# Kernel optimization log

Measured on AMD Instinct MI355X. Metric: run time of the kernel, lower is better.

The kernel has to match this reference:

```python
import jax, jax.numpy as jnp
import numpy as np

H = 1024
S = 2048
B = 16

def setup_inputs() -> dict:
    key = jax.random.key(0)
    k1, k2, k3, k4, k5, k6 = jax.random.split(key, 6)
    hidden = jax.random.normal(k1, (1, B, H), dtype=jnp.float32)
    encoder_outputs = jax.random.normal(k2, (S, B, H), dtype=jnp.float32)
    seq_mask = jax.random.randint(k3, (B, S), 0, 2, dtype=jnp.int32)
    # nn.Linear(2H, H): weight [H, 2H], bias [H]
    lim1 = 1.0 / np.sqrt(2 * H)
    attn_w = jax.random.uniform(k4, (H, 2 * H), minval=-lim1, maxval=lim1, dtype=jnp.float32)
    attn_b = jax.random.uniform(k5, (H,), minval=-lim1, maxval=lim1, dtype=jnp.float32)
    # nn.Linear(H, 1, bias=False): weight [1, H]
    lim2 = 1.0 / np.sqrt(H)
    score_w = jax.random.uniform(k6, (1, H), minval=-lim2, maxval=lim2, dtype=jnp.float32)
    return {"hidden": hidden, "encoder_outputs": encoder_outputs, "seq_mask": seq_mask,
            "attn_w": attn_w, "attn_b": attn_b, "score_w": score_w}

def reference(hidden, encoder_outputs, seq_mask, attn_w, attn_b, score_w):
    # Faithful to: cat([hidden.repeat(S,1,1), encoder_outputs], -1) @ attn_w.T + attn_b
    # Split the concat-linear into two GEMMs (identical math, avoids the big concat).
    h = hidden.shape[-1]
    Wh = attn_w[:, :h]   # acts on repeated hidden
    We = attn_w[:, h:]   # acts on encoder outputs
    # hidden: [1,B,H] broadcasts over S; encoder_outputs: [S,B,H]
    pre = jnp.einsum('obh,kh->obk', hidden, Wh) + jnp.einsum('sbh,kh->sbk', encoder_outputs, We) + attn_b
    proj = jnp.tanh(pre)                               # [S,B,H]
    energies = jnp.einsum('sbh,oh->sbo', proj, score_w)[..., 0]  # [S,B]
    energies = energies.T                              # [B,S] (transpose(0,1) in original)
    energies = jnp.where(seq_mask.astype(bool), jnp.float32(-1e12), energies)
    attn = jax.nn.softmax(energies, axis=1)            # [B,S]
    return attn[:, None, :]                            # [B,1,S]
```

## Files before the change

### kernel.cpp

```cpp
#include <hip/hip_runtime.h>
#include <hip/hip_bf16.h>

#define HDIM 1024
#define SEQ 2048
#define BATCH 16
#define M_TOT (SEQ*BATCH)
#define NBLK 4
#define BM 256
#define BN 256
#define BKT 64
#define NT (HDIM/BKT)

#define NB_ENC ((M_TOT*HDIM)/(8*256))
#define NB_WE  ((HDIM*HDIM)/(8*256))
#define NB_QK  (HDIM)

typedef __attribute__((ext_vector_type(8))) short short8;
typedef __attribute__((ext_vector_type(4))) float f32x4;

typedef const void __attribute__((address_space(1))) gvoid_t;
typedef void __attribute__((address_space(3))) svoid_t;
#define GLD16(gp, lp) __builtin_amdgcn_global_load_lds((gvoid_t*)(gp), (svoid_t*)(lp), 16, 0, 0)
#define VMC(N) asm volatile("s_waitcnt vmcnt(" #N ")" ::: "memory")

static __device__ __forceinline__ unsigned short f2bf(float f) {
    unsigned int x = __float_as_uint(f);
    unsigned int r = (x + 0x7FFFu + ((x >> 16) & 1u)) >> 16;
    return (unsigned short)r;
}

__global__ __launch_bounds__(256) void prep_all(const float* __restrict__ hidden,
                                                const float* __restrict__ enc,
                                                const float* __restrict__ attn_w,
                                                const float* __restrict__ attn_b,
                                                float* __restrict__ q,
                                                __hip_bfloat16* __restrict__ web,
                                                __hip_bfloat16* __restrict__ encb) {
    int bid = blockIdx.x;
    if (bid < NB_ENC) {
        size_t i0 = ((size_t)bid * 256 + threadIdx.x) * 8;
        const float4* s = reinterpret_cast<const float4*>(enc + i0);
        float4 a = s[0], b = s[1];
        union { unsigned short u[8]; short8 v; } cv;
        cv.u[0] = f2bf(a.x); cv.u[1] = f2bf(a.y); cv.u[2] = f2bf(a.z); cv.u[3] = f2bf(a.w);
        cv.u[4] = f2bf(b.x); cv.u[5] = f2bf(b.y); cv.u[6] = f2bf(b.z); cv.u[7] = f2bf(b.w);
        *reinterpret_cast<short8*>((unsigned short*)encb + i0) = cv.v;
        return;
    }
    if (bid < NB_ENC + NB_WE) {
        size_t i0 = ((size_t)(bid - NB_ENC) * 256 + threadIdx.x) * 8;
        int n = (int)(i0 >> 10);
        int h = (int)(i0 & 1023);
        const float4* src = reinterpret_cast<const float4*>(attn_w + (size_t)n * (2 * HDIM) + HDIM + h);
        float4 a = src[0], b = src[1];
        union { unsigned short u[8]; short8 v; } cv;
        cv.u[0] = f2bf(a.x); cv.u[1] = f2bf(a.y); cv.u[2] = f2bf(a.z); cv.u[3] = f2bf(a.w);
        cv.u[4] = f2bf(b.x); cv.u[5] = f2bf(b.y); cv.u[6] = f2bf(b.z); cv.u[7] = f2bf(b.w);
        *reinterpret_cast<short8*>((unsigned short*)web + i0) = cv.v;
        return;
    }
    int k = bid - (NB_ENC + NB_WE);
    int tid = threadIdx.x;
    const float* w = attn_w + (size_t)k * (2 * HDIM);
    float p[BATCH];
#pragma unroll
    for (int b = 0; b < BATCH; b++) p[b] = 0.f;
    for (int h = tid; h < HDIM; h += 256) {
        float wv = w[h];
#pragma unroll
        for (int b = 0; b < BATCH; b++) p[b] += hidden[b * HDIM + h] * wv;
    }
#pragma unroll
    for (int b = 0; b < BATCH; b++) {
        for (int off = 32; off; off >>= 1) p[b] += __shfl_down(p[b], off);
    }
    __shared__ float red[4][BATCH];
    int lane = tid & 63, wid = tid >> 6;
    if (lane == 0) {
#pragma unroll
        for (int b = 0; b < BATCH; b++) red[wid][b] = p[b];
    }
    __syncthreads();
    if (tid < BATCH) {
        float s = red[0][tid] + red[1][tid] + red[2][tid] + red[3][tid] + attn_b[k];
        q[(size_t)tid * HDIM + k] = s;
    }
}

__global__ __launch_bounds__(512, 2) void gemm8(const __hip_bfloat16* __restrict__ encb,
                                                const __hip_bfloat16* __restrict__ web,
                                                const float* __restrict__ qv,
                                                const float* __restrict__ score_w,
                                                float* __restrict__ part) {
    __shared__ __align__(16) char pool[163840];

    int tid = threadIdx.x;
    int lane = tid & 63;
    int wid = tid >> 6;
    int wr = wid >> 2;
    int wc = wid & 3;

    int bid = blockIdx.x;
    int lin = (bid & 7) * 64 + (bid >> 3);
    int bm = lin >> 2;
    int bn = lin & 3;
    int m0 = bm * BM, n0 = bn * BN;

    int srow = tid >> 3;
    int scolb = (((tid & 7) ^ ((tid >> 3) & 7)) << 4);
    const char* eb = (const char*)encb;
    const char* wb = (const char*)web;

    auto STG = [&](const char* g, int ldsoff) {
        GLD16(g + (size_t)srow * 2048 + scolb, pool + ldsoff + wid * 1024);
        GLD16(g + (size_t)(srow + 64) * 2048 + scolb, pool + ldsoff + 8192 + wid * 1024);
    };
    auto APTR = [&](int kt, int h) { return eb + ((size_t)(m0 + h * 128) * HDIM + kt * BKT) * 2; };
    auto BPTR = [&](int kt, int h) { return wb + ((size_t)(n0 + h * 128) * HDIM + kt * BKT) * 2; };
#define ALDS(par, h) ((par) * 32768 + (h) * 16384)
#define BLDS(buf, h) (65536 + (buf) * 32768 + (h) * 16384)

    int lq = lane & 15, lh = lane >> 4;
    int flip = (lane & 7) << 4;
    int pks0 = lq * 128 + ((lh * 16) ^ flip);
    int pks1 = lq * 128 + (((64 + lh * 16)) ^ flip);
    int aFB = wr * 16384;
    int bOFF = (wc >> 1) * 16384 + (wc & 1) * 8192;

    f32x4 acc[8][4];
#pragma unroll
    for (int i = 0; i < 8; i++)
#pragma unroll
        for (int j = 0; j < 4; j++) acc[i][j] = (f32x4)0.f;
    short8 br[4][2];

#define RD8(off) (*reinterpret_cast<const short8*>(pool + (off)))

#define CLUSTER(Q, PAR, BB, STAGE_STMT)                                                   \
    {                                                                                     \
        if ((Q) == 0) {                                                                   \
            _Pragma("unroll") for (int nj = 0; nj < 4; ++nj) {                            \
                br[nj][0] = RD8(65536 + (BB) * 32768 + bOFF + nj * 2048 + pks0);          \
                br[nj][1] = RD8(65536 + (BB) * 32768 + bOFF + nj * 2048 + pks1);          \
            }                                                                             \
        }                                                                                 \
        short8 a0k0 = RD8(aFB + (PAR) * 32768 + (2 * (Q)) * 2048 + pks0);                 \
        short8 a0k1 = RD8(aFB + (PAR) * 32768 + (2 * (Q)) * 2048 + pks1);                 \
        short8 a1k0 = RD8(aFB + (PAR) * 32768 + (2 * (Q) + 1) * 2048 + pks0);             \
        short8 a1k1 = RD8(aFB + (PAR) * 32768 + (2 * (Q) + 1) * 2048 + pks1);             \
        STAGE_STMT;                                                                       \
        __builtin_amdgcn_s_setprio(1);                                                    \
        _Pragma("unroll") for (int nj = 0; nj < 4; ++nj) {                                \
            acc[2 * (Q)][nj] = __builtin_amdgcn_mfma_f32_16x16x32_bf16(a0k0, br[nj][0], acc[2 * (Q)][nj], 0, 0, 0); \
            acc[2 * (Q)][nj] = __builtin_amdgcn_mfma_f32_16x16x32_bf16(a0k1, br[nj][1], acc[2 * (Q)][nj], 0, 0, 0); \
            acc[2 * (Q) + 1][nj] = __builtin_amdgcn_mfma_f32_16x16x32_bf16(a1k0, br[nj][0], acc[2 * (Q) + 1][nj], 0, 0, 0); \
            acc[2 * (Q) + 1][nj] = __builtin_amdgcn_mfma_f32_16x16x32_bf16(a1k1, br[nj][1], acc[2 * (Q) + 1][nj], 0, 0, 0); \
        }                                                                                 \
        __builtin_amdgcn_s_setprio(0);                                                    \
    }

#define TILE(PAR, BB, S1, S2, S3, S4, CLOSE)                                              \
    {                                                                                     \
        CLUSTER(0, PAR, BB, S1);                                                          \
        CLUSTER(1, PAR, BB, S2);                                                          \
        CLUSTER(2, PAR, BB, S3);                                                          \
        CLUSTER(3, PAR, BB, S4);                                                          \
        CLOSE;                                                                            \
        __builtin_amdgcn_s_barrier();                                                     \
        __builtin_amdgcn_sched_barrier(0);                                                \
    }

    STG(APTR(0, 0), ALDS(0, 0));
    STG(APTR(0, 1), ALDS(0, 1));
    STG(BPTR(0, 0), BLDS(0, 0));
    STG(BPTR(0, 1), BLDS(0, 1));
    STG(BPTR(1, 0), BLDS(1, 0));
    STG(BPTR(1, 1), BLDS(1, 1));
    VMC(4);
    __builtin_amdgcn_s_barrier();
    __builtin_amdgcn_sched_barrier(0);

#pragma unroll 1
    for (int J = 0; J < 2; ++J) {
        int t = 6 * J;
        TILE(0, 0, STG(APTR(t + 1, 0), ALDS(1, 0)), STG(APTR(t + 1, 1), ALDS(1, 1)),
                   STG(BPTR(t + 2, 0), BLDS(2, 0)), STG(BPTR(t + 2, 1), BLDS(2, 1)), VMC(4));
        TILE(1, 1, STG(APTR(t + 2, 0), ALDS(0, 0)), STG(APTR(t + 2, 1), ALDS(0, 1)),
                   STG(BPTR(t + 3, 0), BLDS(0, 0)), STG(BPTR(t + 3, 1), BLDS(0, 1)), VMC(4));
        TILE(0, 2, STG(APTR(t + 3, 0), ALDS(1, 0)), STG(APTR(t + 3, 1), ALDS(1, 1)),
                   STG(BPTR(t + 4, 0), BLDS(1, 0)), STG(BPTR(t + 4, 1), BLDS(1, 1)), VMC(4));
        TILE(1, 0, STG(APTR(t + 4, 0), ALDS(0, 0)), STG(APTR(t + 4, 1), ALDS(0, 1)),
                   STG(BPTR(t + 5, 0), BLDS(2, 0)), STG(BPTR(t + 5, 1), BLDS(2, 1)), VMC(4));
        TILE(0, 1, STG(APTR(t + 5, 0), ALDS(1, 0)), STG(APTR(t + 5, 1), ALDS(1, 1)),
                   STG(BPTR(t + 6, 0), BLDS(0, 0)), STG(BPTR(t + 6, 1), BLDS(0, 1)), VMC(4));
        TILE(1, 2, STG(APTR(t + 6, 0), ALDS(0, 0)), STG(APTR(t + 6, 1), ALDS(0, 1)),
                   STG(BPTR(t + 7, 0), BLDS(1, 0)), STG(BPTR(t + 7, 1), BLDS(1, 1)), VMC(4));
    }
    TILE(0, 0, STG(APTR(13, 0), ALDS(1, 0)), STG(APTR(13, 1), ALDS(1, 1)),
               STG(BPTR(14, 0), BLDS(2, 0)), STG(BPTR(14, 1), BLDS(2, 1)), VMC(4));
    TILE(1, 1, STG(APTR(14, 0), ALDS(0, 0)), STG(APTR(14, 1), ALDS(0, 1)),
               STG(BPTR(15, 0), BLDS(0, 0)), STG(BPTR(15, 1), BLDS(0, 1)), VMC(4));
    TILE(0, 2, STG(APTR(15, 0), ALDS(1, 0)), STG(APTR(15, 1), ALDS(1, 1)), , , VMC(0));
    TILE(1, 0, , , , , );

    float* q_lds = reinterpret_cast<float*>(pool);
    float* sc_lds = reinterpret_cast<float*>(pool + 16384);
    float* eng = reinterpret_cast<float*>(pool + 17408);
    {
        int qb = tid >> 5;
        int kl = (tid & 31) * 8;
        const float4* src = reinterpret_cast<const float4*>(qv + (size_t)qb * HDIM + n0 + kl);
        float4 v0 = src[0], v1 = src[1];
        *reinterpret_cast<float4*>(&q_lds[qb * 256 + kl]) = v0;
        *reinterpret_cast<float4*>(&q_lds[qb * 256 + kl + 4]) = v1;
        if (tid < BN) sc_lds[tid] = score_w[n0 + tid];
    }
    __syncthreads();

#pragma unroll
    for (int mi = 0; mi < 8; ++mi) {
#pragma unroll
        for (int r = 0; r < 4; ++r) {
            int b = lh * 4 + r;
            float s = 0.f;
#pragma unroll
            for (int nj = 0; nj < 4; ++nj) {
                int kl = wc * 64 + nj * 16 + lq;
                float v = acc[mi][nj][r] + q_lds[b * 256 + kl];
                float t = 1.f - 2.f / (__expf(2.f * v) + 1.f);
                s += sc_lds[kl] * t;
            }
            for (int off = 1; off < 16; off <<= 1) s += __shfl_xor(s, off);
            if (lq == 0) eng[wc * 256 + wr * 128 + mi * 16 + b] = s;
        }
    }
    __syncthreads();
    if (tid < BM) {
        float s = eng[tid] + eng[256 + tid] + eng[512 + tid] + eng[768 + tid];
        part[(size_t)bn * M_TOT + m0 + tid] = s;
    }
#undef CLUSTER
#undef TILE
#undef RD8
#undef ALDS
#undef BLDS
}

__global__ __launch_bounds__(256) void softmax_kernel(const float* __restrict__ part,
                                                      const int* __restrict__ mask,
                                                      float* __restrict__ out) {
    int b = blockIdx.x;
    int tid = threadIdx.x;
    __shared__ float e_lds[SEQ];
    __shared__ float red[4], red2[4];
    int lane = tid & 63, wid = tid >> 6;
    float lmax = -3.4e38f;
    for (int it = 0; it < SEQ / 256; ++it) {
        int s = it * 256 + tid;
        size_t m = (size_t)s * BATCH + b;
        float e = 0.f;
#pragma unroll
        for (int c = 0; c < NBLK; c++) e += part[(size_t)c * M_TOT + m];
        if (mask[(size_t)b * SEQ + s]) e = -1e12f;
        e_lds[s] = e;
        lmax = fmaxf(lmax, e);
    }
    for (int off = 32; off; off >>= 1) lmax = fmaxf(lmax, __shfl_xor(lmax, off));
    if (lane == 0) red[wid] = lmax;
    __syncthreads();
    float gmax = fmaxf(fmaxf(red[0], red[1]), fmaxf(red[2], red[3]));
    float lsum = 0.f;
    for (int it = 0; it < SEQ / 256; ++it) {
        int s = it * 256 + tid;
        float p = __expf(e_lds[s] - gmax);
        e_lds[s] = p;
        lsum += p;
    }
    for (int off = 32; off; off >>= 1) lsum += __shfl_xor(lsum, off);
    if (lane == 0) red2[wid] = lsum;
    __syncthreads();
    float inv = 1.f / (red2[0] + red2[1] + red2[2] + red2[3]);
    for (int it = 0; it < SEQ / 256; ++it) {
        int s = it * 256 + tid;
        out[(size_t)b * SEQ + s] = e_lds[s] * inv;
    }
}

extern "C" void kernel_launch(void* const* d_in, const int* in_sizes, int n_in,
                              void* d_out, int out_size, void* d_ws, size_t ws_size,
                              hipStream_t stream) {
    const float* hidden   = (const float*)d_in[0];
    const float* enc      = (const float*)d_in[1];
    const int*   seq_mask = (const int*)d_in[2];
    const float* attn_w   = (const float*)d_in[3];
    const float* attn_b   = (const float*)d_in[4];
    const float* score_w  = (const float*)d_in[5];
    float* out = (float*)d_out;

    char* ws = (char*)d_ws;
    float* q = (float*)ws;
    __hip_bfloat16* web = (__hip_bfloat16*)(ws + 65536);
    float* part = (float*)(ws + 65536 + 2 * 1024 * 1024);
    __hip_bfloat16* encb = (__hip_bfloat16*)(ws + 65536 + 3 * 1024 * 1024);

    prep_all<<<dim3(NB_ENC + NB_WE + NB_QK), dim3(256), 0, stream>>>(hidden, enc, attn_w, attn_b, q, web, encb);
    gemm8<<<dim3(NBLK * (M_TOT / BM)), dim3(512), 0, stream>>>(encb, web, q, score_w, part);
    softmax_kernel<<<dim3(BATCH), dim3(256), 0, stream>>>(part, seq_mask, out);
}
```

Measured before the change: 118.6 us.

## Fuse fp32-to-bf16 encoder conversion into GEMM A-tile loading

Drops the separate pass that converts encoder_outputs to a bf16 workspace copy. The GEMM now loads fp32 A tiles into registers, converts them to bf16 and writes them into swizzled LDS, and keeps the async global-to-LDS path only for the weight tiles. This removes a full write and re-read of the 64MB bf16 copy. BM is halved to 128 and the grid doubled, so each block holds fewer accumulators and uses less LDS. The cost is more register pressure and extra VALU conversion work inside the main loop, and weight tiles are reused less per block.

```diff
diff --git a/kernel.cpp b/kernel.cpp
--- a/kernel.cpp
+++ b/kernel.cpp
@@ -6,12 +6,11 @@
 #define BATCH 16
 #define M_TOT (SEQ*BATCH)
 #define NBLK 4
-#define BM 256
+#define BM 128
 #define BN 256
 #define BKT 64
 #define NT (HDIM/BKT)
 
-#define NB_ENC ((M_TOT*HDIM)/(8*256))
 #define NB_WE  ((HDIM*HDIM)/(8*256))
 #define NB_QK  (HDIM)
 
@@ -22,6 +21,7 @@
 typedef void __attribute__((address_space(3))) svoid_t;
 #define GLD16(gp, lp) __builtin_amdgcn_global_load_lds((gvoid_t*)(gp), (svoid_t*)(lp), 16, 0, 0)
 #define VMC(N) asm volatile("s_waitcnt vmcnt(" #N ")" ::: "memory")
+#define LGKM0 asm volatile("s_waitcnt lgkmcnt(0)" ::: "memory")
 
 static __device__ __forceinline__ unsigned short f2bf(float f) {
     unsigned int x = __float_as_uint(f);
@@ -30,25 +30,13 @@
 }
 
 __global__ __launch_bounds__(256) void prep_all(const float* __restrict__ hidden,
-                                                const float* __restrict__ enc,
                                                 const float* __restrict__ attn_w,
                                                 const float* __restrict__ attn_b,
                                                 float* __restrict__ q,
-                                                __hip_bfloat16* __restrict__ web,
-                                                __hip_bfloat16* __restrict__ encb) {
+                                                __hip_bfloat16* __restrict__ web) {
     int bid = blockIdx.x;
-    if (bid < NB_ENC) {
+    if (bid < NB_WE) {
         size_t i0 = ((size_t)bid * 256 + threadIdx.x) * 8;
-        const float4* s = reinterpret_cast<const float4*>(enc + i0);
-        float4 a = s[0], b = s[1];
-        union { unsigned short u[8]; short8 v; } cv;
-        cv.u[0] = f2bf(a.x); cv.u[1] = f2bf(a.y); cv.u[2] = f2bf(a.z); cv.u[3] = f2bf(a.w);
-        cv.u[4] = f2bf(b.x); cv.u[5] = f2bf(b.y); cv.u[6] = f2bf(b.z); cv.u[7] = f2bf(b.w);
-        *reinterpret_cast<short8*>((unsigned short*)encb + i0) = cv.v;
-        return;
-    }
-    if (bid < NB_ENC + NB_WE) {
-        size_t i0 = ((size_t)(bid - NB_ENC) * 256 + threadIdx.x) * 8;
         int n = (int)(i0 >> 10);
         int h = (int)(i0 & 1023);
         const float4* src = reinterpret_cast<const float4*>(attn_w + (size_t)n * (2 * HDIM) + HDIM + h);
@@ -59,7 +47,7 @@
         *reinterpret_cast<short8*>((unsigned short*)web + i0) = cv.v;
         return;
     }
-    int k = bid - (NB_ENC + NB_WE);
+    int k = bid - NB_WE;
     int tid = threadIdx.x;
     const float* w = attn_w + (size_t)k * (2 * HDIM);
     float p[BATCH];
@@ -87,12 +75,12 @@
     }
 }
 
-__global__ __launch_bounds__(512, 2) void gemm8(const __hip_bfloat16* __restrict__ encb,
+__global__ __launch_bounds__(512, 2) void gemmf(const float* __restrict__ enc,
                                                 const __hip_bfloat16* __restrict__ web,
                                                 const float* __restrict__ qv,
                                                 const float* __restrict__ score_w,
                                                 float* __restrict__ part) {
-    __shared__ __align__(16) char pool[163840];
+    __shared__ __align__(16) char pool[131072];
 
     int tid = threadIdx.x;
     int lane = tid & 63;
@@ -101,107 +89,119 @@
     int wc = wid & 3;
 
     int bid = blockIdx.x;
-    int lin = (bid & 7) * 64 + (bid >> 3);
+    int lin = (bid & 7) * 128 + (bid >> 3);
     int bm = lin >> 2;
     int bn = lin & 3;
     int m0 = bm * BM, n0 = bn * BN;
 
     int srow = tid >> 3;
     int scolb = (((tid & 7) ^ ((tid >> 3) & 7)) << 4);
-    const char* eb = (const char*)encb;
     const char* wb = (const char*)web;
-
     auto STG = [&](const char* g, int ldsoff) {
         GLD16(g + (size_t)srow * 2048 + scolb, pool + ldsoff + wid * 1024);
         GLD16(g + (size_t)(srow + 64) * 2048 + scolb, pool + ldsoff + 8192 + wid * 1024);
     };
-    auto APTR = [&](int kt, int h) { return eb + ((size_t)(m0 + h * 128) * HDIM + kt * BKT) * 2; };
     auto BPTR = [&](int kt, int h) { return wb + ((size_t)(n0 + h * 128) * HDIM + kt * BKT) * 2; };
-#define ALDS(par, h) ((par) * 32768 + (h) * 16384)
-#define BLDS(buf, h) (65536 + (buf) * 32768 + (h) * 16384)
+#define BLDS(buf, h) (32768 + (buf) * 32768 + (h) * 16384)
+    auto BSTG = [&](int kt, int buf) { STG(BPTR(kt, 0), BLDS(buf, 0)); STG(BPTR(kt, 1), BLDS(buf, 1)); };
+
+    int arow = tid >> 2;
+    int a4 = tid & 3;
+    int ar7 = arow & 7;
+    int s0b = ((a4 * 2) ^ ar7) << 4;
+    int s1b = ((a4 * 2 + 1) ^ ar7) << 4;
+    float4 av0[4], av1[4];
+    auto ALD = [&](int kt, float4* av) {
+        const float4* p = reinterpret_cast<const float4*>(enc + (size_t)(m0 + arow) * HDIM + kt * BKT + a4 * 16);
+        av[0] = p[0]; av[1] = p[1]; av[2] = p[2]; av[3] = p[3];
+    };
+    auto CVT2 = [&](float4 lo, float4 hi) {
+        union { __hip_bfloat162 b[4]; short8 s; } u;
+        u.b[0] = __float22bfloat162_rn(make_float2(lo.x, lo.y));
+        u.b[1] = __float22bfloat162_rn(make_float2(lo.z, lo.w));
+        u.b[2] = __float22bfloat162_rn(make_float2(hi.x, hi.y));
+        u.b[3] = __float22bfloat162_rn(make_float2(hi.z, hi.w));
+        return u.s;
+    };
+    auto AWR = [&](float4* av, int par) {
+        short8 w0 = CVT2(av[0], av[1]);
+        short8 w1 = CVT2(av[2], av[3]);
+        char* base = pool + par * 16384 + arow * 128;
+        *reinterpret_cast<short8*>(base + s0b) = w0;
+        *reinterpret_cast<short8*>(base + s1b) = w1;
+    };
 
     int lq = lane & 15, lh = lane >> 4;
-    int flip = (lane & 7) << 4;
+    int flip = (lq & 7) << 4;
     int pks0 = lq * 128 + ((lh * 16) ^ flip);
-    int pks1 = lq * 128 + (((64 + lh * 16)) ^ flip);
-    int aFB = wr * 16384;
-    int bOFF = (wc >> 1) * 16384 + (wc & 1) * 8192;
-
-    f32x4 acc[8][4];
-#pragma unroll
-    for (int i = 0; i < 8; i++)
+    int pks1 = lq * 128 + ((64 + lh * 16) ^ flip);
+    int aFB = wr * 8192;
+    int bFB = 32768 + wc * 8192;
+
+    f32x4 acc[4][4];
+#pragma unroll
+    for (int i = 0; i < 4; i++)
 #pragma unroll
         for (int j = 0; j < 4; j++) acc[i][j] = (f32x4)0.f;
     short8 br[4][2];
 
 #define RD8(off) (*reinterpret_cast<const short8*>(pool + (off)))
 
-#define CLUSTER(Q, PAR, BB, STAGE_STMT)                                                   \
+#define CLUSTER(MI, PAR, BB, STAGE_STMT)                                                  \
     {                                                                                     \
-        if ((Q) == 0) {                                                                   \
+        if ((MI) == 0) {                                                                  \
             _Pragma("unroll") for (int nj = 0; nj < 4; ++nj) {                            \
-                br[nj][0] = RD8(65536 + (BB) * 32768 + bOFF + nj * 2048 + pks0);          \
-                br[nj][1] = RD8(65536 + (BB) * 32768 + bOFF + nj * 2048 + pks1);          \
+                br[nj][0] = RD8(bFB + (BB) * 32768 + nj * 2048 + pks0);                   \
+                br[nj][1] = RD8(bFB + (BB) * 32768 + nj * 2048 + pks1);                   \
             }                                                                             \
         }                                                                                 \
-        short8 a0k0 = RD8(aFB + (PAR) * 32768 + (2 * (Q)) * 2048 + pks0);                 \
-        short8 a0k1 = RD8(aFB + (PAR) * 32768 + (2 * (Q)) * 2048 + pks1);                 \
-        short8 a1k0 = RD8(aFB + (PAR) * 32768 + (2 * (Q) + 1) * 2048 + pks0);             \
-        short8 a1k1 = RD8(aFB + (PAR) * 32768 + (2 * (Q) + 1) * 2048 + pks1);             \
+        short8 ak0 = RD8(aFB + (PAR) * 16384 + (MI) * 2048 + pks0);                       \
+        short8 ak1 = RD8(aFB + (PAR) * 16384 + (MI) * 2048 + pks1);                       \
         STAGE_STMT;                                                                       \
         __builtin_amdgcn_s_setprio(1);                                                    \
         _Pragma("unroll") for (int nj = 0; nj < 4; ++nj) {                                \
-            acc[2 * (Q)][nj] = __builtin_amdgcn_mfma_f32_16x16x32_bf16(a0k0, br[nj][0], acc[2 * (Q)][nj], 0, 0, 0); \
-            acc[2 * (Q)][nj] = __builtin_amdgcn_mfma_f32_16x16x32_bf16(a0k1, br[nj][1], acc[2 * (Q)][nj], 0, 0, 0); \
-            acc[2 * (Q) + 1][nj] = __builtin_amdgcn_mfma_f32_16x16x32_bf16(a1k0, br[nj][0], acc[2 * (Q) + 1][nj], 0, 0, 0); \
-            acc[2 * (Q) + 1][nj] = __builtin_amdgcn_mfma_f32_16x16x32_bf16(a1k1, br[nj][1], acc[2 * (Q) + 1][nj], 0, 0, 0); \
+            acc[MI][nj] = __builtin_amdgcn_mfma_f32_16x16x32_bf16(ak0, br[nj][0], acc[MI][nj], 0, 0, 0); \
+            acc[MI][nj] = __builtin_amdgcn_mfma_f32_16x16x32_bf16(ak1, br[nj][1], acc[MI][nj], 0, 0, 0); \
         }                                                                                 \
         __builtin_amdgcn_s_setprio(0);                                                    \
     }
 
-#define TILE(PAR, BB, S1, S2, S3, S4, CLOSE)                                              \
+#define TILE(PAR, BB, S1, S2, S3)                                                         \
     {                                                                                     \
         CLUSTER(0, PAR, BB, S1);                                                          \
         CLUSTER(1, PAR, BB, S2);                                                          \
         CLUSTER(2, PAR, BB, S3);                                                          \
-        CLUSTER(3, PAR, BB, S4);                                                          \
-        CLOSE;                                                                            \
+        CLUSTER(3, PAR, BB, );                                                            \
+        LGKM0;                                                                            \
         __builtin_amdgcn_s_barrier();                                                     \
         __builtin_amdgcn_sched_barrier(0);                                                \
     }
 
-    STG(APTR(0, 0), ALDS(0, 0));
-    STG(APTR(0, 1), ALDS(0, 1));
-    STG(BPTR(0, 0), BLDS(0, 0));
-    STG(BPTR(0, 1), BLDS(0, 1));
-    STG(BPTR(1, 0), BLDS(1, 0));
-    STG(BPTR(1, 1), BLDS(1, 1));
-    VMC(4);
+    ALD(0, av0);
+    BSTG(0, 0);
+    BSTG(1, 1);
+    VMC(8);
+    AWR(av0, 0);
+    ALD(1, av1);
+    VMC(8);
+    LGKM0;
     __builtin_amdgcn_s_barrier();
     __builtin_amdgcn_sched_barrier(0);
 
 #pragma unroll 1
     for (int J = 0; J < 2; ++J) {
         int t = 6 * J;
-        TILE(0, 0, STG(APTR(t + 1, 0), ALDS(1, 0)), STG(APTR(t + 1, 1), ALDS(1, 1)),
-                   STG(BPTR(t + 2, 0), BLDS(2, 0)), STG(BPTR(t + 2, 1), BLDS(2, 1)), VMC(4));
-        TILE(1, 1, STG(APTR(t + 2, 0), ALDS(0, 0)), STG(APTR(t + 2, 1), ALDS(0, 1)),
-                   STG(BPTR(t + 3, 0), BLDS(0, 0)), STG(BPTR(t + 3, 1), BLDS(0, 1)), VMC(4));
-        TILE(0, 2, STG(APTR(t + 3, 0), ALDS(1, 0)), STG(APTR(t + 3, 1), ALDS(1, 1)),
-                   STG(BPTR(t + 4, 0), BLDS(1, 0)), STG(BPTR(t + 4, 1), BLDS(1, 1)), VMC(4));
-        TILE(1, 0, STG(APTR(t + 4, 0), ALDS(0, 0)), STG(APTR(t + 4, 1), ALDS(0, 1)),
-                   STG(BPTR(t + 5, 0), BLDS(2, 0)), STG(BPTR(t + 5, 1), BLDS(2, 1)), VMC(4));
-        TILE(0, 1, STG(APTR(t + 5, 0), ALDS(1, 0)), STG(APTR(t + 5, 1), ALDS(1, 1)),
-                   STG(BPTR(t + 6, 0), BLDS(0, 0)), STG(BPTR(t + 6, 1), BLDS(0, 1)), VMC(4));
-        TILE(1, 2, STG(APTR(t + 6, 0), ALDS(0, 0)), STG(APTR(t + 6, 1), ALDS(0, 1)),
-                   STG(BPTR(t + 7, 0), BLDS(1, 0)), STG(BPTR(t + 7, 1), BLDS(1, 1)), VMC(4));
-    }
-    TILE(0, 0, STG(APTR(13, 0), ALDS(1, 0)), STG(APTR(13, 1), ALDS(1, 1)),
-               STG(BPTR(14, 0), BLDS(2, 0)), STG(BPTR(14, 1), BLDS(2, 1)), VMC(4));
-    TILE(1, 1, STG(APTR(14, 0), ALDS(0, 0)), STG(APTR(14, 1), ALDS(0, 1)),
-               STG(BPTR(15, 0), BLDS(0, 0)), STG(BPTR(15, 1), BLDS(0, 1)), VMC(4));
-    TILE(0, 2, STG(APTR(15, 0), ALDS(1, 0)), STG(APTR(15, 1), ALDS(1, 1)), , , VMC(0));
-    TILE(1, 0, , , , , );
+        TILE(0, 0, ALD(t + 2, av0), BSTG(t + 2, 2), { VMC(8); AWR(av1, 1); });
+        TILE(1, 1, ALD(t + 3, av1), BSTG(t + 3, 0), { VMC(8); AWR(av0, 0); });
+        TILE(0, 2, ALD(t + 4, av0), BSTG(t + 4, 1), { VMC(8); AWR(av1, 1); });
+        TILE(1, 0, ALD(t + 5, av1), BSTG(t + 5, 2), { VMC(8); AWR(av0, 0); });
+        TILE(0, 1, ALD(t + 6, av0), BSTG(t + 6, 0), { VMC(8); AWR(av1, 1); });
+        TILE(1, 2, ALD(t + 7, av1), BSTG(t + 7, 1), { VMC(8); AWR(av0, 0); });
+    }
+    TILE(0, 0, ALD(14, av0), BSTG(14, 2), { VMC(8); AWR(av1, 1); });
+    TILE(1, 1, ALD(15, av1), BSTG(15, 0), { VMC(8); AWR(av0, 0); });
+    TILE(0, 2, , , { VMC(0); AWR(av1, 1); });
+    TILE(1, 0, , , );
 
     float* q_lds = reinterpret_cast<float*>(pool);
     float* sc_lds = reinterpret_cast<float*>(pool + 16384);
@@ -218,7 +218,7 @@
     __syncthreads();
 
 #pragma unroll
-    for (int mi = 0; mi < 8; ++mi) {
+    for (int mi = 0; mi < 4; ++mi) {
 #pragma unroll
         for (int r = 0; r < 4; ++r) {
             int b = lh * 4 + r;
@@ -231,18 +231,17 @@
                 s += sc_lds[kl] * t;
             }
             for (int off = 1; off < 16; off <<= 1) s += __shfl_xor(s, off);
-            if (lq == 0) eng[wc * 256 + wr * 128 + mi * 16 + b] = s;
+            if (lq == 0) eng[wc * 128 + wr * 64 + mi * 16 + b] = s;
         }
     }
     __syncthreads();
     if (tid < BM) {
-        float s = eng[tid] + eng[256 + tid] + eng[512 + tid] + eng[768 + tid];
+        float s = eng[tid] + eng[128 + tid] + eng[256 + tid] + eng[384 + tid];
         part[(size_t)bn * M_TOT + m0 + tid] = s;
     }
 #undef CLUSTER
 #undef TILE
 #undef RD8
-#undef ALDS
 #undef BLDS
 }
 
@@ -301,9 +300,8 @@
     float* q = (float*)ws;
     __hip_bfloat16* web = (__hip_bfloat16*)(ws + 65536);
     float* part = (float*)(ws + 65536 + 2 * 1024 * 1024);
-    __hip_bfloat16* encb = (__hip_bfloat16*)(ws + 65536 + 3 * 1024 * 1024);
-
-    prep_all<<<dim3(NB_ENC + NB_WE + NB_QK), dim3(256), 0, stream>>>(hidden, enc, attn_w, attn_b, q, web, encb);
-    gemm8<<<dim3(NBLK * (M_TOT / BM)), dim3(512), 0, stream>>>(encb, web, q, score_w, part);
+
+    prep_all<<<dim3(NB_WE + NB_QK), dim3(256), 0, stream>>>(hidden, attn_w, attn_b, q, web);
+    gemmf<<<dim3(NBLK * (M_TOT / BM)), dim3(512), 0, stream>>>(enc, web, q, score_w, part);
     softmax_kernel<<<dim3(BATCH), dim3(256), 0, stream>>>(part, seq_mask, out);
 }
```

Result: slower. 130.0 us (+9.6%).
